# Performance work log

Hardware: AMD Instinct MI355X
Metric: run time of the kernel (lower is better)

Reference implementation:

```python
import jax, jax.numpy as jnp
import numpy as np
import math

IN_FEATURES = 4096
OUT_FEATURES = 4096
P = max(IN_FEATURES, OUT_FEATURES)   # total_permutations
D = min(IN_FEATURES, OUT_FEATURES)   # diag_length
SPARSITY = 0.1
K = math.ceil(int((1.0 - SPARSITY) * IN_FEATURES * OUT_FEATURES) / D)  # 3687
ALPHA_LR = 0.01
NUM_ITER = 50


def sparse_soft_topk_mask_dykstra(alpha, k, l, num_iter):
    """Dykstra projection of alpha/l onto {0<=m<=1, sum(m)=k} (soft top-k mask)."""
    s = alpha / l
    n = s.shape[0]
    p0 = jnp.zeros_like(s)
    q0 = jnp.zeros_like(s)

    def body(carry, _):
        x, p, q = carry
        # project x+p onto hyperplane sum = k
        t = x + p
        y = t + (k - jnp.sum(t)) / n
        p = t - y
        # project y+q onto box [0, 1]
        u = y + q
        x_new = jnp.clip(u, 0.0, 1.0)
        q = u - x_new
        return (x_new, p, q), None

    (x, _, _), _ = jax.lax.scan(body, (s, p0, q0), None, length=num_iter)
    return x  # last projection is onto the box -> exact zeros / ones


def compute_weight(V, alpha):
    a = sparse_soft_topk_mask_dykstra(alpha, K, ALPHA_LR, NUM_ITER)  # (P,)
    vals = a[:, None] * V                                             # (P, D)
    i = jnp.arange(P)[:, None]
    j = jnp.arange(D)[None, :]
    if OUT_FEATURES >= IN_FEATURES:
        # pseudo-diagonal i: rows shifted by i, column j scaled by V[i, j]
        rows = (i + j) % OUT_FEATURES
        cols = jnp.broadcast_to(j, (P, D))
    else:
        # row r scaled by V[i, r], columns shifted by i
        rows = jnp.broadcast_to(j, (P, D))
        cols = (i + j) % IN_FEATURES
    W = jnp.zeros((OUT_FEATURES, IN_FEATURES), V.dtype)
    W = W.at[rows.reshape(-1), cols.reshape(-1)].add(vals.reshape(-1))
    return W


def setup_inputs() -> dict:
    key = jax.random.key(0)
    k1, k2 = jax.random.split(key)
    # kaiming_uniform_(a=sqrt(5)) over fan_in = D -> bound = sqrt(1/D)
    bound = 1.0 / np.sqrt(D)
    V = jax.random.uniform(k1, (P, D), jnp.float32, -bound, bound)
    alpha = jnp.ones((P,), jnp.float32) / IN_FEATURES
    x = jax.random.normal(k2, (512, IN_FEATURES), jnp.float32)
    return {"x": x, "V": V, "alpha": alpha}


def reference(x, V, alpha):
    W = compute_weight(V, alpha)  # (out, in)
    return x @ W.T                # F.linear(x, W)
```

## Files before the change

kernel.cpp:

```cpp
#include <hip/hip_runtime.h>
#include <hip/hip_bf16.h>
#include <stdint.h>

#define PDIM 4096
#define KSEL 3687.0f
#define NITER 50

typedef unsigned short ushort_t;
typedef __attribute__((ext_vector_type(8))) __bf16 bf16x8;
typedef __attribute__((ext_vector_type(4))) float f32x4;

typedef __attribute__((address_space(3))) void lds_void;
typedef __attribute__((address_space(1))) const void glob_void;

__device__ __forceinline__ ushort_t f32_to_bf16_rne(float f) {
  union { float f; uint32_t u; } v; v.f = f;
  uint32_t r = 0x7FFFu + ((v.u >> 16) & 1u);
  return (ushort_t)((v.u + r) >> 16);
}

__device__ __forceinline__ float bf16_to_f32(ushort_t h) {
  union { uint32_t u; float f; } v; v.u = ((uint32_t)h) << 16;
  return v.f;
}

__device__ __forceinline__ void async_cp16(const void* g, void* l) {
  __builtin_amdgcn_global_load_lds((glob_void*)g, (lds_void*)l, 16, 0, 0);
}

__device__ __forceinline__ float wave_sum_dpp(float x) {
  float s = x;
  int t;
  t = __builtin_amdgcn_update_dpp(0, __float_as_int(s), 0x111, 0xF, 0xF, true);
  s += __int_as_float(t);
  t = __builtin_amdgcn_update_dpp(0, __float_as_int(s), 0x112, 0xF, 0xF, true);
  s += __int_as_float(t);
  t = __builtin_amdgcn_update_dpp(0, __float_as_int(s), 0x114, 0xF, 0xF, true);
  s += __int_as_float(t);
  t = __builtin_amdgcn_update_dpp(0, __float_as_int(s), 0x118, 0xF, 0xF, true);
  s += __int_as_float(t);
  t = __builtin_amdgcn_update_dpp(0, __float_as_int(s), 0x142, 0xA, 0xF, true);
  s += __int_as_float(t);
  t = __builtin_amdgcn_update_dpp(0, __float_as_int(s), 0x143, 0xC, 0xF, true);
  s += __int_as_float(t);
  return s;
}

__global__ __launch_bounds__(256) void prep_kernel(
    const float* __restrict__ alpha, float* __restrict__ a_out,
    const float* __restrict__ x, ushort_t* __restrict__ Xb, int n4,
    const float* __restrict__ V) {
  if (blockIdx.x >= 1 && blockIdx.x <= 2048) {
    const float4* V4 = (const float4*)V;
    const int base = (blockIdx.x - 1) * 2048 + (int)threadIdx.x;
#pragma unroll
    for (int i = 0; i < 8; ++i) {
      const float4 vv = V4[base + i * 256];
      asm volatile("" :: "v"(vv.x), "v"(vv.y), "v"(vv.z), "v"(vv.w));
    }
    return;
  }
  if (blockIdx.x != 0) {
    const int i = (blockIdx.x - 2049) * 256 + threadIdx.x;
    if (i < n4) {
      const float4 v = ((const float4*)x)[i];
      ushort4 o;
      o.x = f32_to_bf16_rne(v.x);
      o.y = f32_to_bf16_rne(v.y);
      o.z = f32_to_bf16_rne(v.z);
      o.w = f32_to_bf16_rne(v.w);
      ((ushort4*)Xb)[i] = o;
    }
    return;
  }
  __shared__ float red[8];
  const int tid = threadIdx.x;
  const int lane = tid & 63;
  const int wv = tid >> 6;
  float xx[16], q[16];
  float p = 0.0f;
#pragma unroll
  for (int i = 0; i < 16; ++i) {
    xx[i] = alpha[i * 256 + tid] * 100.0f;
    q[i] = 0.0f;
  }
  for (int it = 0; it < NITER; ++it) {
    float t[16];
    float loc = 0.0f;
#pragma unroll
    for (int i = 0; i < 16; ++i) { t[i] = xx[i] + p; loc += t[i]; }
    loc = wave_sum_dpp(loc);
    const int slot = (it & 1) * 4;
    if (lane == 63) red[slot + wv] = loc;
    __syncthreads();
    const float tot = red[slot] + red[slot + 1] + red[slot + 2] + red[slot + 3];
    const float corr = (KSEL - tot) * (1.0f / 4096.0f);
    p = -corr;
#pragma unroll
    for (int i = 0; i < 16; ++i) {
      const float y = t[i] + corr;
      const float u = y + q[i];
      const float xn = fminf(fmaxf(u, 0.0f), 1.0f);
      q[i] = u - xn;
      xx[i] = xn;
    }
  }
#pragma unroll
  for (int i = 0; i < 16; ++i) a_out[i * 256 + tid] = xx[i];
}

__global__ __launch_bounds__(256) void wmat_kernel(
    const float* __restrict__ V, const float* __restrict__ a,
    ushort_t* __restrict__ Wb) {
  __shared__ float vt[192][67];
  const int t = threadIdx.x;
  const int r0 = blockIdx.x * 128;
  const int c0 = blockIdx.y * 64;
  const int dbase = (r0 - c0 - 63 + 2 * PDIM) & (PDIM - 1);
  const int csub = (t & 15) * 4;
  const int rsub = t >> 4;
#pragma unroll
  for (int i = 0; i < 12; ++i) {
    const int ld = i * 16 + rsub;
    const int d = (dbase + ld) & (PDIM - 1);
    const float av = a[d];
    const float4 vv = *(const float4*)(V + (size_t)d * PDIM + c0 + csub);
    vt[ld][csub + 0] = av * vv.x;
    vt[ld][csub + 1] = av * vv.y;
    vt[ld][csub + 2] = av * vv.z;
    vt[ld][csub + 3] = av * vv.w;
  }
  __syncthreads();
#pragma unroll
  for (int k = 0; k < 4; ++k) {
    const int ry = (t >> 3) + k * 32;
    const int cb = (t & 7) * 8;
    ushort_t pk[8];
#pragma unroll
    for (int j = 0; j < 8; ++j) {
      const int c = cb + j;
      pk[j] = f32_to_bf16_rne(vt[ry - c + 63][c]);
    }
    *(uint4*)(Wb + (size_t)(r0 + ry) * PDIM + c0 + cb) = *(const uint4*)pk;
  }
}

__global__ __launch_bounds__(256, 3) void gemm_kernel(
    const ushort_t* __restrict__ Xb, const ushort_t* __restrict__ Wb,
    ushort_t* __restrict__ par) {
  constexpr int Kdim = 4096, KQ = 1024;
  __shared__ __align__(16) ushort_t As[128 * 64];
  __shared__ __align__(16) ushort_t Bs[128 * 64];
  const int tid = threadIdx.x;
  const int lane = tid & 63;
  const int w = tid >> 6;
  const int l15 = lane & 15;
  const int quad = lane >> 4;
  const int bid = blockIdx.x;
  const int u = ((bid & 7) << 6) | (bid >> 3);
  const int z = u & 3;
  const int mblk = (u >> 2) & 3;
  const int nblk = u >> 4;
  const int m0 = mblk * 128;
  const int n0 = nblk * 128;
  const int kbase = z * KQ;
  const int arow = lane >> 3;
  const int aslot = lane & 7;

  f32x4 acc[8][2];
#pragma unroll
  for (int mt = 0; mt < 8; ++mt)
#pragma unroll
    for (int nt = 0; nt < 2; ++nt) acc[mt][nt] = (f32x4){0.f, 0.f, 0.f, 0.f};

  for (int it = 0; it < KQ / 64; ++it) {
    const int k0 = kbase + it * 64;
#pragma unroll
    for (int s = w; s < 16; s += 4) {
      const int row = s * 8 + arow;
      const int j = aslot ^ (row & 7);
      async_cp16(Xb + (size_t)(m0 + row) * Kdim + k0 + j * 8,
                 (char*)As + (size_t)s * 1024);
      async_cp16(Wb + (size_t)(n0 + row) * Kdim + k0 + j * 8,
                 (char*)Bs + (size_t)s * 1024);
    }
    __syncthreads();
#pragma unroll
    for (int kk = 0; kk < 64; kk += 32) {
      const int cj = (kk >> 3) + quad;
      bf16x8 bfv[2];
#pragma unroll
      for (int nt = 0; nt < 2; ++nt) {
        const int row = w * 32 + nt * 16 + l15;
        bfv[nt] = *(const bf16x8*)&Bs[(row * 8 + (cj ^ (row & 7))) * 8];
      }
#pragma unroll
      for (int mt = 0; mt < 8; ++mt) {
        const int row = mt * 16 + l15;
        const bf16x8 af = *(const bf16x8*)&As[(row * 8 + (cj ^ (row & 7))) * 8];
        acc[mt][0] = __builtin_amdgcn_mfma_f32_16x16x32_bf16(af, bfv[0],
                                                             acc[mt][0], 0, 0, 0);
        acc[mt][1] = __builtin_amdgcn_mfma_f32_16x16x32_bf16(af, bfv[1],
                                                             acc[mt][1], 0, 0, 0);
      }
    }
    __syncthreads();
  }
  const int tile = nblk * 4 + mblk;
  ushort_t* pbase = par + ((size_t)z * 128 + tile) * 16384;
#pragma unroll
  for (int mt = 0; mt < 8; ++mt) {
#pragma unroll
    for (int nt = 0; nt < 2; ++nt) {
      const int slot = mt * 2 + nt;
      ushort4 o;
      o.x = f32_to_bf16_rne(acc[mt][nt][0]);
      o.y = f32_to_bf16_rne(acc[mt][nt][1]);
      o.z = f32_to_bf16_rne(acc[mt][nt][2]);
      o.w = f32_to_bf16_rne(acc[mt][nt][3]);
      *(ushort4*)(pbase + (size_t)(slot * 256 + tid) * 4) = o;
    }
  }
}

__global__ __launch_bounds__(256) void combine_kernel(
    const ushort_t* __restrict__ par, float* __restrict__ out) {
  const int tile = blockIdx.x >> 2;
  const int qh = blockIdx.x & 3;
  const int nblk = tile >> 2;
  const int mblk = tile & 3;
  const int m0 = mblk * 128;
  const int n0 = nblk * 128;
  const int tid = threadIdx.x;
  const int lane = tid & 63;
  const int w = tid >> 6;
  const int l15 = lane & 15;
  const int quad = lane >> 4;
#pragma unroll
  for (int ss = 0; ss < 4; ++ss) {
    const int slot = qh * 4 + ss;
    float s0 = 0.f, s1 = 0.f, s2 = 0.f, s3 = 0.f;
#pragma unroll
    for (int z = 0; z < 4; ++z) {
      const ushort4 v = *(const ushort4*)(par +
          ((size_t)z * 128 + tile) * 16384 + (size_t)(slot * 256 + tid) * 4);
      s0 += bf16_to_f32(v.x);
      s1 += bf16_to_f32(v.y);
      s2 += bf16_to_f32(v.z);
      s3 += bf16_to_f32(v.w);
    }
    const int mt = slot >> 1;
    const int nt = slot & 1;
    const int mb = m0 + mt * 16 + quad * 4;
    const int n = n0 + w * 32 + nt * 16 + l15;
    out[(size_t)(mb + 0) * PDIM + n] = s0;
    out[(size_t)(mb + 1) * PDIM + n] = s1;
    out[(size_t)(mb + 2) * PDIM + n] = s2;
    out[(size_t)(mb + 3) * PDIM + n] = s3;
  }
}

extern "C" void kernel_launch(void* const* d_in, const int* in_sizes, int n_in,
                              void* d_out, int out_size, void* d_ws,
                              size_t ws_size, hipStream_t stream) {
  const float* x = (const float*)d_in[0];
  const float* V = (const float*)d_in[1];
  const float* alpha = (const float*)d_in[2];
  float* out = (float*)d_out;
  const int M = in_sizes[0] / PDIM;

  float* a_mask = (float*)d_ws;
  ushort_t* Xb = (ushort_t*)((char*)d_ws + 16 * 1024);
  ushort_t* Wb = Xb + (size_t)M * PDIM;
  ushort_t* par = Wb + (size_t)PDIM * PDIM;

  const int n4x = (M * PDIM) / 4;
  prep_kernel<<<1 + 2048 + (n4x + 255) / 256, 256, 0, stream>>>(
      alpha, a_mask, x, Xb, n4x, V);
  wmat_kernel<<<dim3(PDIM / 128, PDIM / 64), 256, 0, stream>>>(V, a_mask, Wb);
  gemm_kernel<<<512, 256, 0, stream>>>(Xb, Wb, par);
  combine_kernel<<<512, 256, 0, stream>>>(par, out);
}
```

Before: 149.7 us.

## Fuse Dykstra mask, weight build, and x cast into one flag-synchronized kernel

Rewrites the Dykstra iteration to track only a scalar shift c, so the mask becomes clip(s+c) and each block can recompute its slice of the mask locally. The prep and weight-materialization kernels are merged into one launch. Weight-tile blocks load V into LDS first, then spin on a global flag published by block 0 with release/acquire semantics, and fall back to computing c themselves if the flag times out. This removes a kernel boundary and the separate V-prefetch pass, at the cost of an extra tiny zero kernel, spin-waiting, and a risk of redundant Dykstra work if block 0 is scheduled late.

```diff
diff --git a/kernel.cpp b/kernel.cpp
--- a/kernel.cpp
+++ b/kernel.cpp
@@ -5,6 +5,7 @@
 #define PDIM 4096
 #define KSEL 3687.0f
 #define NITER 50
+#define FLAG_READY 0x5A17C0DE
 
 typedef unsigned short ushort_t;
 typedef __attribute__((ext_vector_type(8))) __bf16 bf16x8;
@@ -46,102 +47,127 @@
   return s;
 }
 
-__global__ __launch_bounds__(256) void prep_kernel(
-    const float* __restrict__ alpha, float* __restrict__ a_out,
-    const float* __restrict__ x, ushort_t* __restrict__ Xb, int n4,
-    const float* __restrict__ V) {
-  if (blockIdx.x >= 1 && blockIdx.x <= 2048) {
-    const float4* V4 = (const float4*)V;
-    const int base = (blockIdx.x - 1) * 2048 + (int)threadIdx.x;
-#pragma unroll
-    for (int i = 0; i < 8; ++i) {
-      const float4 vv = V4[base + i * 256];
-      asm volatile("" :: "v"(vv.x), "v"(vv.y), "v"(vv.z), "v"(vv.w));
-    }
-    return;
-  }
-  if (blockIdx.x != 0) {
-    const int i = (blockIdx.x - 2049) * 256 + threadIdx.x;
-    if (i < n4) {
-      const float4 v = ((const float4*)x)[i];
-      ushort4 o;
-      o.x = f32_to_bf16_rne(v.x);
-      o.y = f32_to_bf16_rne(v.y);
-      o.z = f32_to_bf16_rne(v.z);
-      o.w = f32_to_bf16_rne(v.w);
-      ((ushort4*)Xb)[i] = o;
-    }
-    return;
-  }
-  __shared__ float red[8];
-  const int tid = threadIdx.x;
+__device__ float dykstra_c(const float* __restrict__ alpha, float* red,
+                           int tid) {
   const int lane = tid & 63;
   const int wv = tid >> 6;
-  float xx[16], q[16];
-  float p = 0.0f;
-#pragma unroll
-  for (int i = 0; i < 16; ++i) {
-    xx[i] = alpha[i * 256 + tid] * 100.0f;
-    q[i] = 0.0f;
-  }
+  float s[16];
+#pragma unroll
+  for (int i = 0; i < 16; ++i) s[i] = alpha[i * 256 + tid] * 100.0f;
+  float c = 0.0f;
   for (int it = 0; it < NITER; ++it) {
-    float t[16];
     float loc = 0.0f;
 #pragma unroll
-    for (int i = 0; i < 16; ++i) { t[i] = xx[i] + p; loc += t[i]; }
+    for (int i = 0; i < 16; ++i) {
+      const float v = fminf(fmaxf(s[i] + c, 0.0f), 1.0f);
+      loc += v;
+    }
     loc = wave_sum_dpp(loc);
     const int slot = (it & 1) * 4;
     if (lane == 63) red[slot + wv] = loc;
     __syncthreads();
     const float tot = red[slot] + red[slot + 1] + red[slot + 2] + red[slot + 3];
-    const float corr = (KSEL - tot) * (1.0f / 4096.0f);
-    p = -corr;
-#pragma unroll
-    for (int i = 0; i < 16; ++i) {
-      const float y = t[i] + corr;
-      const float u = y + q[i];
-      const float xn = fminf(fmaxf(u, 0.0f), 1.0f);
-      q[i] = u - xn;
-      xx[i] = xn;
-    }
-  }
-#pragma unroll
-  for (int i = 0; i < 16; ++i) a_out[i * 256 + tid] = xx[i];
-}
-
-__global__ __launch_bounds__(256) void wmat_kernel(
-    const float* __restrict__ V, const float* __restrict__ a,
-    ushort_t* __restrict__ Wb) {
+    c += (KSEL - tot) * (1.0f / 4096.0f);
+  }
+  return c;
+}
+
+__global__ void zero_kernel(int* __restrict__ flag) {
+  if (threadIdx.x == 0) flag[0] = 0;
+}
+
+__global__ __launch_bounds__(256) void fused_kernel(
+    const float* __restrict__ alpha, const float* __restrict__ V,
+    const float* __restrict__ x, ushort_t* __restrict__ Xb, int n4,
+    ushort_t* __restrict__ Wb, float* __restrict__ csl,
+    int* __restrict__ flag) {
   __shared__ float vt[192][67];
-  const int t = threadIdx.x;
-  const int r0 = blockIdx.x * 128;
-  const int c0 = blockIdx.y * 64;
-  const int dbase = (r0 - c0 - 63 + 2 * PDIM) & (PDIM - 1);
-  const int csub = (t & 15) * 4;
-  const int rsub = t >> 4;
-#pragma unroll
-  for (int i = 0; i < 12; ++i) {
-    const int ld = i * 16 + rsub;
-    const int d = (dbase + ld) & (PDIM - 1);
-    const float av = a[d];
-    const float4 vv = *(const float4*)(V + (size_t)d * PDIM + c0 + csub);
-    vt[ld][csub + 0] = av * vv.x;
-    vt[ld][csub + 1] = av * vv.y;
-    vt[ld][csub + 2] = av * vv.z;
-    vt[ld][csub + 3] = av * vv.w;
-  }
-  __syncthreads();
-#pragma unroll
-  for (int k = 0; k < 4; ++k) {
-    const int ry = (t >> 3) + k * 32;
-    const int cb = (t & 7) * 8;
-    ushort_t pk[8];
-#pragma unroll
-    for (int j = 0; j < 8; ++j) {
-      const int c = cb + j;
-      pk[j] = f32_to_bf16_rne(vt[ry - c + 63][c]);
-    }
-    *(uint4*)(Wb + (size_t)(r0 + ry) * PDIM + c0 + cb) = *(const uint4*)pk;
+  __shared__ float a_lds[192];
+  __shared__ float cbc[2];
+  __shared__ float red[8];
+  const int bid = blockIdx.x;
+  const int tid = threadIdx.x;
+
+  if (bid == 0) {
+    const float c = dykstra_c(alpha, red, tid);
+    if (tid == 0) {
+      csl[0] = c;
+      __hip_atomic_store(flag, FLAG_READY, __ATOMIC_RELEASE,
+                         __HIP_MEMORY_SCOPE_AGENT);
+    }
+    return;
+  }
+
+  if (bid <= 2048) {
+    const int tile = bid - 1;
+    const int bx = tile & 31;
+    const int by = tile >> 5;
+    const int r0 = bx * 128;
+    const int c0 = by * 64;
+    const int dbase = (r0 - c0 - 63 + 2 * PDIM) & (PDIM - 1);
+    const int csub = (tid & 15) * 4;
+    const int rsub = tid >> 4;
+#pragma unroll
+    for (int i = 0; i < 12; ++i) {
+      const int ld = i * 16 + rsub;
+      const int d = (dbase + ld) & (PDIM - 1);
+      const float4 vv = *(const float4*)(V + (size_t)d * PDIM + c0 + csub);
+      vt[ld][csub + 0] = vv.x;
+      vt[ld][csub + 1] = vv.y;
+      vt[ld][csub + 2] = vv.z;
+      vt[ld][csub + 3] = vv.w;
+    }
+    if (tid == 0) {
+      float cv = 0.0f, ok = 0.0f;
+      for (int sp = 0; sp < 100000; ++sp) {
+        if (__hip_atomic_load(flag, __ATOMIC_ACQUIRE,
+                              __HIP_MEMORY_SCOPE_AGENT) == FLAG_READY) {
+          cv = csl[0];
+          ok = 1.0f;
+          break;
+        }
+        __builtin_amdgcn_s_sleep(8);
+      }
+      cbc[0] = cv;
+      cbc[1] = ok;
+    }
+    __syncthreads();
+    float c;
+    if (cbc[1] != 0.0f) {
+      c = cbc[0];
+    } else {
+      c = dykstra_c(alpha, red, tid);
+    }
+    if (tid < 192) {
+      const int d = (dbase + tid) & (PDIM - 1);
+      a_lds[tid] = fminf(fmaxf(alpha[d] * 100.0f + c, 0.0f), 1.0f);
+    }
+    __syncthreads();
+#pragma unroll
+    for (int k = 0; k < 4; ++k) {
+      const int ry = (tid >> 3) + k * 32;
+      const int cb = (tid & 7) * 8;
+      ushort_t pk[8];
+#pragma unroll
+      for (int j = 0; j < 8; ++j) {
+        const int cc = cb + j;
+        const int ld = ry - cc + 63;
+        pk[j] = f32_to_bf16_rne(a_lds[ld] * vt[ld][cc]);
+      }
+      *(uint4*)(Wb + (size_t)(r0 + ry) * PDIM + c0 + cb) = *(const uint4*)pk;
+    }
+    return;
+  }
+
+  const int i = (bid - 2049) * 256 + tid;
+  if (i < n4) {
+    const float4 v = ((const float4*)x)[i];
+    ushort4 o;
+    o.x = f32_to_bf16_rne(v.x);
+    o.y = f32_to_bf16_rne(v.y);
+    o.z = f32_to_bf16_rne(v.z);
+    o.w = f32_to_bf16_rne(v.w);
+    ((ushort4*)Xb)[i] = o;
   }
 }
 
@@ -269,15 +295,16 @@
   float* out = (float*)d_out;
   const int M = in_sizes[0] / PDIM;
 
-  float* a_mask = (float*)d_ws;
+  float* csl = (float*)d_ws;
+  int* flag = (int*)d_ws + 4;
   ushort_t* Xb = (ushort_t*)((char*)d_ws + 16 * 1024);
   ushort_t* Wb = Xb + (size_t)M * PDIM;
   ushort_t* par = Wb + (size_t)PDIM * PDIM;
 
   const int n4x = (M * PDIM) / 4;
-  prep_kernel<<<1 + 2048 + (n4x + 255) / 256, 256, 0, stream>>>(
-      alpha, a_mask, x, Xb, n4x, V);
-  wmat_kernel<<<dim3(PDIM / 128, PDIM / 64), 256, 0, stream>>>(V, a_mask, Wb);
+  zero_kernel<<<1, 64, 0, stream>>>(flag);
+  fused_kernel<<<1 + 2048 + 2048, 256, 0, stream>>>(alpha, V, x, Xb, n4x, Wb,
+                                                    csl, flag);
   gemm_kernel<<<512, 256, 0, stream>>>(Xb, Wb, par);
   combine_kernel<<<512, 256, 0, stream>>>(par, out);
 }
```

New measurement: 165.8 us. 1.11x slower.

## Double-buffer LDS tiles in GEMM with async prefetch of next K-slice

Applied to the files above, without the earlier changes.

The GEMM main loop now keeps two LDS buffers per operand. It issues the async global-to-LDS loads for the next K step before computing on the current one, and waits with a partial vmcnt so that global load latency overlaps MFMA work. Plain __syncthreads is replaced by raw s_barrier calls wrapped in scheduling fences. LDS use doubles, so the occupancy hint drops from 3 to 2 blocks per CU. The vmcnt(8) value depends on each thread issuing exactly 8 loads per stage.

```diff
diff --git a/kernel.cpp b/kernel.cpp
--- a/kernel.cpp
+++ b/kernel.cpp
@@ -26,6 +26,14 @@
 
 __device__ __forceinline__ void async_cp16(const void* g, void* l) {
   __builtin_amdgcn_global_load_lds((glob_void*)g, (lds_void*)l, 16, 0, 0);
+}
+
+__device__ __forceinline__ void raw_barrier() {
+  __builtin_amdgcn_sched_barrier(0);
+  asm volatile("" ::: "memory");
+  __builtin_amdgcn_s_barrier();
+  asm volatile("" ::: "memory");
+  __builtin_amdgcn_sched_barrier(0);
 }
 
 __device__ __forceinline__ float wave_sum_dpp(float x) {
@@ -145,12 +153,12 @@
   }
 }
 
-__global__ __launch_bounds__(256, 3) void gemm_kernel(
+__global__ __launch_bounds__(256, 2) void gemm_kernel(
     const ushort_t* __restrict__ Xb, const ushort_t* __restrict__ Wb,
     ushort_t* __restrict__ par) {
-  constexpr int Kdim = 4096, KQ = 1024;
-  __shared__ __align__(16) ushort_t As[128 * 64];
-  __shared__ __align__(16) ushort_t Bs[128 * 64];
+  constexpr int Kdim = 4096, KQ = 1024, NIT = KQ / 64;
+  __shared__ __align__(16) ushort_t As[2][128 * 64];
+  __shared__ __align__(16) ushort_t Bs[2][128 * 64];
   const int tid = threadIdx.x;
   const int lane = tid & 63;
   const int w = tid >> 6;
@@ -173,18 +181,31 @@
 #pragma unroll
     for (int nt = 0; nt < 2; ++nt) acc[mt][nt] = (f32x4){0.f, 0.f, 0.f, 0.f};
 
-  for (int it = 0; it < KQ / 64; ++it) {
+  auto stage = [&](int buf, int it) {
     const int k0 = kbase + it * 64;
 #pragma unroll
     for (int s = w; s < 16; s += 4) {
       const int row = s * 8 + arow;
       const int j = aslot ^ (row & 7);
       async_cp16(Xb + (size_t)(m0 + row) * Kdim + k0 + j * 8,
-                 (char*)As + (size_t)s * 1024);
+                 (char*)&As[buf][0] + (size_t)s * 1024);
       async_cp16(Wb + (size_t)(n0 + row) * Kdim + k0 + j * 8,
-                 (char*)Bs + (size_t)s * 1024);
-    }
-    __syncthreads();
+                 (char*)&Bs[buf][0] + (size_t)s * 1024);
+    }
+  };
+
+  stage(0, 0);
+  for (int it = 0; it < NIT; ++it) {
+    const int cur = it & 1;
+    if (it < NIT - 1) {
+      stage(cur ^ 1, it + 1);
+      asm volatile("s_waitcnt vmcnt(8)" ::: "memory");
+    } else {
+      asm volatile("s_waitcnt vmcnt(0)" ::: "memory");
+    }
+    raw_barrier();
+    const ushort_t* __restrict__ Ab = &As[cur][0];
+    const ushort_t* __restrict__ Bb = &Bs[cur][0];
 #pragma unroll
     for (int kk = 0; kk < 64; kk += 32) {
       const int cj = (kk >> 3) + quad;
@@ -192,19 +213,19 @@
 #pragma unroll
       for (int nt = 0; nt < 2; ++nt) {
         const int row = w * 32 + nt * 16 + l15;
-        bfv[nt] = *(const bf16x8*)&Bs[(row * 8 + (cj ^ (row & 7))) * 8];
+        bfv[nt] = *(const bf16x8*)&Bb[(row * 8 + (cj ^ (row & 7))) * 8];
       }
 #pragma unroll
       for (int mt = 0; mt < 8; ++mt) {
         const int row = mt * 16 + l15;
-        const bf16x8 af = *(const bf16x8*)&As[(row * 8 + (cj ^ (row & 7))) * 8];
+        const bf16x8 af = *(const bf16x8*)&Ab[(row * 8 + (cj ^ (row & 7))) * 8];
         acc[mt][0] = __builtin_amdgcn_mfma_f32_16x16x32_bf16(af, bfv[0],
                                                              acc[mt][0], 0, 0, 0);
         acc[mt][1] = __builtin_amdgcn_mfma_f32_16x16x32_bf16(af, bfv[1],
                                                              acc[mt][1], 0, 0, 0);
       }
     }
-    __syncthreads();
+    raw_barrier();
   }
   const int tile = nblk * 4 + mblk;
   ushort_t* pbase = par + ((size_t)z * 128 + tile) * 16384;
```

Measured after the change: 149.9 us. Within noise of the previous version (+0.1%).
